# Kernel tuning notes

Measured on AMD Instinct MI355X. Metric: run time of the kernel, lower is better.

Reference implementation:

```python
import jax, jax.numpy as jnp
import numpy as np
from jax.scipy.special import gammaln

# NQ_IN + 4 == 2*H is required because the two kernel=1, padding=1 convs grow the
# length axis by 4 and the following nn.Linear(2H, H) acts on the length axis.
B, NQ_IN, NK, QDIM, KDIM, H = 16, 2044, 1024, 80, 256, 1024


def setup_inputs() -> dict:
    ks = jax.random.split(jax.random.key(0), 14)
    s = 0.02
    return {
        "query": jax.random.normal(ks[0], (B, NQ_IN, QDIM), jnp.float32),
        "key": jax.random.normal(ks[1], (B, NK, KDIM), jnp.float32),
        "query_lens": jnp.full((B,), 2 * H, jnp.int32),
        "key_lens": jnp.full((B,), NK, jnp.int32),
        # query branch params (Conv1d k=1 stored as (out,in); Linear as (out,in))
        "qc1_w": jax.random.normal(ks[2], (2 * H, QDIM), jnp.float32) * s,
        "qc1_b": jax.random.normal(ks[3], (2 * H,), jnp.float32) * s,
        "qc2_w": jax.random.normal(ks[4], (2 * H, 2 * H), jnp.float32) * s,
        "qc2_b": jax.random.normal(ks[5], (2 * H,), jnp.float32) * s,
        "ql_w": jax.random.normal(ks[6], (H, 2 * H), jnp.float32) * s,
        "ql_b": jax.random.normal(ks[7], (H,), jnp.float32) * s,
        # key branch params
        "kc_w": jax.random.normal(ks[8], (H, KDIM, 3), jnp.float32) * s,
        "kc_b": jax.random.normal(ks[9], (H,), jnp.float32) * s,
        "kl1_w": jax.random.normal(ks[10], (2 * H, H), jnp.float32) * s,
        "kl1_b": jax.random.normal(ks[11], (2 * H,), jnp.float32) * s,
        "kl2_w": jax.random.normal(ks[12], (H, 2 * H), jnp.float32) * s,
        "kl2_b": jax.random.normal(ks[13], (H,), jnp.float32) * s,
    }


def _log_beta_binom(query_lens, key_lens, tq, tk):
    # Standard MAS beta-binomial alignment prior over a (tq, tk) grid.
    i = jnp.arange(tq, dtype=jnp.float32)[None, :, None]
    j = jnp.arange(tk, dtype=jnp.float32)[None, None, :]
    ql = query_lens.astype(jnp.float32)[:, None, None]
    kl = key_lens.astype(jnp.float32)[:, None, None]
    a = i + 1.0
    b = jnp.maximum(ql - i, 1.0)
    n = jnp.maximum(kl - 1.0, 0.0)
    nmj = jnp.maximum(n - j, 0.0)

    def betaln(x, y):
        return gammaln(x) + gammaln(y) - gammaln(x + y)

    logp = (gammaln(n + 1.0) - gammaln(j + 1.0) - gammaln(nmj + 1.0)
            + betaln(j + a, nmj + b) - betaln(a, b))
    valid = (i < ql) & (j < kl)
    return jnp.where(valid, logp, -1e9)


def _forward(query, key, query_lens, key_lens,
             qc1_w, qc1_b, qc2_w, qc2_b, ql_w, ql_b,
             kc_w, kc_b, kl1_w, kl1_b, kl2_w, kl2_b):
    # query branch: b n c -> b c n, two k=1/p=1 convs (pad length, pointwise), Linear over LENGTH axis
    q = jnp.transpose(query, (0, 2, 1))                       # (B, QDIM, NQ_IN)
    q = jnp.pad(q, ((0, 0), (0, 0), (1, 1)))
    q = jnp.einsum('bcn,oc->bon', q, qc1_w) + qc1_b[None, :, None]   # (B, 2H, NQ_IN+2)
    q = jnp.pad(q, ((0, 0), (0, 0), (1, 1)))
    q = jnp.einsum('bcn,oc->bon', q, qc2_w) + qc2_b[None, :, None]   # (B, 2H, 2H)
    q = jnp.einsum('bcn,hn->bch', q, ql_w) + ql_b                    # (B, 2H, H) Linear on length axis

    # key branch: b n c -> b c n, Conv1d k=3 p=1, then two Linears over LENGTH axis
    k = jnp.transpose(key, (0, 2, 1))                         # (B, KDIM, NK)
    k = jax.lax.conv_general_dilated(k, kc_w, (1,), ((1, 1),),
                                     dimension_numbers=('NCH', 'OIH', 'NCH'))
    k = k + kc_b[None, :, None]                               # (B, H, NK=H)
    k = jnp.einsum('bcn,on->bco', k, kl1_w) + kl1_b           # (B, H, 2H)
    k = jnp.einsum('bco,ho->bch', k, kl2_w) + kl2_b           # (B, H, H)

    # dist = -cdist(q, k), computed via the GEMM form (same as torch.cdist mm mode)
    sq = (jnp.sum(q * q, -1)[:, :, None] + jnp.sum(k * k, -1)[:, None, :]
          - 2.0 * jnp.einsum('bnd,bmd->bnm', q, k))           # (B, 2H, H)
    dist = -jnp.sqrt(jnp.maximum(sq, 1e-12))

    prior = _log_beta_binom(query_lens, key_lens, q.shape[1], k.shape[1])
    return jax.nn.log_softmax(dist + prior, axis=-1)


def reference(query, key, query_lens, key_lens,
              qc1_w, qc1_b, qc2_w, qc2_b, ql_w, ql_b,
              kc_w, kc_b, kl1_w, kl1_b, kl2_w, kl2_b):
    return _forward(query, key, query_lens, key_lens,
                    qc1_w, qc1_b, qc2_w, qc2_b, ql_w, ql_b,
                    kc_w, kc_b, kl1_w, kl1_b, kl2_w, kl2_b)
```

## Files before the change

### kernel.cpp

```cpp
#include <hip/hip_runtime.h>
#include <math.h>

typedef unsigned short u16;
typedef float floatx4 __attribute__((ext_vector_type(4)));
typedef __bf16 bf16x8 __attribute__((ext_vector_type(8)));

#define BB   16
#define TQ   2048
#define TK   1024
#define HH   1024
#define H2   2048
#define QD   80
#define QDP  128
#define KD   256
#define NQ   2044
#define NKEY 1024
#define T12N 3072

__device__ __forceinline__ u16 f2bf(float f) {
  unsigned int u = __float_as_uint(f);
  u = u + 0x7fffu + ((u >> 16) & 1u);
  return (u16)(u >> 16);
}
__device__ __forceinline__ float bf2f(u16 s) {
  return __uint_as_float(((unsigned int)s) << 16);
}
__device__ __forceinline__ float tgf(const float* __restrict__ tbl, int x) {
  return tbl[(x < 8191) ? (x < 0 ? 0 : x) : 8191];
}

__global__ __launch_bounds__(256) void prep_all_k(
    const float* __restrict__ qc2_w, const float* __restrict__ kl2_w,
    const float* __restrict__ ql_w, const float* __restrict__ kc_w,
    const float* __restrict__ kl1_w,
    u16* __restrict__ qc2w, u16* __restrict__ kl2w, u16* __restrict__ qlw2,
    u16* __restrict__ kcp, float* __restrict__ colsum1, float* __restrict__ tbl)
{
  long b = blockIdx.x;
  const int t = threadIdx.x;
  __shared__ float red[256];
  if (b < 16384) {
    long i = b * 256 + t; qc2w[i] = f2bf(qc2_w[i]); return;
  }
  b -= 16384;
  if (b < 8192) {
    long i = b * 256 + t; kl2w[i] = f2bf(kl2_w[i]); return;
  }
  b -= 8192;
  if (b < 8192) {
    long i = b * 256 + t;
    int n = (int)(i & 2047);
    int h = (int)(i >> 11);
    qlw2[i] = (n < NQ) ? f2bf(ql_w[(long)h * H2 + n + 2]) : (u16)0; return;
  }
  b -= 8192;
  if (b < 3072) {
    long i = b * 256 + t;
    int r = (int)(i % 768);
    int o = (int)(i / 768);
    int tt = r >> 8, d = r & 255;
    kcp[i] = f2bf(kc_w[((long)o * KD + d) * 3 + tt]); return;
  }
  b -= 3072;
  if (b < 2048) {
    const float* row = kl1_w + b * (long)HH;
    float s = row[t] + row[t + 256] + row[t + 512] + row[t + 768];
    red[t] = s; __syncthreads();
    for (int st = 128; st > 0; st >>= 1) { if (t < st) red[t] += red[t + st]; __syncthreads(); }
    if (!t) colsum1[b] = red[0];
    return;
  }
  b -= 2048;
  { int i = (int)(b * 256 + t); if (i < 8192) tbl[i] = i ? (float)lgamma((double)i) : 0.0f; }
}

__global__ __launch_bounds__(256) void tpack_k(
    const float* __restrict__ kl1_w, const float* __restrict__ qc1_w,
    const float* __restrict__ query,
    u16* __restrict__ kl1T, u16* __restrict__ qc1T, u16* __restrict__ qT)
{
  __shared__ float tile[64][65];
  int bid = blockIdx.x;
  const int tid = threadIdx.x;
  const int r4 = tid >> 6, c = tid & 63;
  const float* src; u16* dst;
  int sr0, sc0, srcR, srcC, srcStride, dstC;
  if (bid < 512) {
    sr0 = (bid >> 4) * 64; sc0 = (bid & 15) * 64;
    src = kl1_w; srcR = 2048; srcC = 1024; srcStride = 1024;
    dst = kl1T; dstC = 2048;
  } else if ((bid -= 512) < 64) {
    sr0 = (bid >> 1) * 64; sc0 = (bid & 1) * 64;
    src = qc1_w; srcR = 2048; srcC = QD; srcStride = QD;
    dst = qc1T; dstC = 2048;
  } else {
    bid -= 64;
    const int b16 = bid >> 6, r = bid & 63;
    sr0 = (r >> 1) * 64; sc0 = (r & 1) * 64;
    src = query + (long)b16 * NQ * QD; srcR = NQ; srcC = QD; srcStride = QD;
    dst = qT + (long)b16 * QDP * 2048; dstC = 2048;
  }
#pragma unroll
  for (int rr = r4; rr < 64; rr += 4) {
    const int gr = sr0 + rr, gc = sc0 + c;
    tile[rr][c] = (gr < srcR && gc < srcC) ? src[(long)gr * srcStride + gc] : 0.f;
  }
  __syncthreads();
#pragma unroll
  for (int rr = r4; rr < 64; rr += 4)
    dst[(long)(sc0 + rr) * dstC + sr0 + c] = f2bf(tile[c][rr]);
}

__global__ __launch_bounds__(256) void pack_kcolT_k(const float* __restrict__ key, u16* __restrict__ out) {
  __shared__ float tile[64][65];
  const int bid = blockIdx.x, tid = threadIdx.x;
  const int b = bid >> 6, r = bid & 63;
  const int m0 = (r >> 2) * 64;
  const int d0 = (r & 3) * 64;
  const int r4 = tid >> 6, c = tid & 63;
#pragma unroll
  for (int rr = r4; rr < 64; rr += 4)
    tile[rr][c] = key[((long)b * NKEY + m0 + rr) * KD + d0 + c];
  __syncthreads();
#pragma unroll
  for (int t = 0; t < 3; t++) {
    const int n = m0 + 1 - t + c;
    if (n >= 0 && n < NKEY) {
#pragma unroll
      for (int rr = r4; rr < 64; rr += 4)
        out[((long)b * 768 + t * 256 + d0 + rr) * NKEY + n] = f2bf(tile[c][rr]);
    }
  }
  if (m0 == 0 && c == 0) {
#pragma unroll
    for (int rr = r4; rr < 64; rr += 4)
      out[((long)b * 768 + d0 + rr) * NKEY + 0] = (u16)0;
  }
  if (m0 == 960 && c == 0) {
#pragma unroll
    for (int rr = r4; rr < 64; rr += 4)
      out[((long)b * 768 + 512 + d0 + rr) * NKEY + (NKEY - 1)] = (u16)0;
  }
}

__global__ __launch_bounds__(256) void fold_bias_k(
    const float* __restrict__ qc2_w, const float* __restrict__ qc1_b, const float* __restrict__ qc2_b,
    const float* __restrict__ kl2_w, const float* __restrict__ kl1_b, const float* __restrict__ kl2_b,
    const float* __restrict__ ql_w, const float* __restrict__ colsum1,
    float* __restrict__ bqm, float* __restrict__ bkv, float* __restrict__ s1v, float* __restrict__ s0v,
    float* __restrict__ wsum)
{
  const int bid = blockIdx.x, t = threadIdx.x;
  float s = 0.f, s2 = 0.f;
  if (bid < H2) {
    const float* row = qc2_w + (long)bid * H2;
    for (int k = t; k < H2; k += 256) s += row[k] * qc1_b[k];
  } else if (bid < H2 + HH) {
    const float* row = kl2_w + (long)(bid - H2) * H2;
    for (int k = t; k < H2; k += 256) { const float rv = row[k]; s += rv * kl1_b[k]; s2 += rv * colsum1[k]; }
  } else {
    const float* row = ql_w + (long)(bid - H2 - HH) * H2;
    for (int m = 1 + t; m <= H2 - 2; m += 256) s += row[m];
  }
  __shared__ float red[256];
  __shared__ float red2[256];
  red[t] = s; red2[t] = s2; __syncthreads();
  for (int st = 128; st > 0; st >>= 1) {
    if (t < st) { red[t] += red[t + st]; red2[t] += red2[t + st]; }
    __syncthreads();
  }
  if (!t) {
    if (bid < H2) bqm[bid] = red[0] + qc2_b[bid];
    else if (bid < H2 + HH) { bkv[bid - H2] = red[0] + kl2_b[bid - H2]; wsum[bid - H2] = red2[0]; }
    else {
      int h = bid - H2 - HH;
      s1v[h] = red[0];
      s0v[h] = ql_w[(long)h * H2] + ql_w[(long)h * H2 + H2 - 1];
    }
  }
}

__device__ __forceinline__ void gld_lds16(const u16* g, u16* l) {
  __builtin_amdgcn_global_load_lds((const __attribute__((address_space(1))) void*)g,
                                   (__attribute__((address_space(3))) void*)l, 16, 0, 0);
}

template<int OUTF32>
__global__ __launch_bounds__(256) void gemm_bt(
    const u16* __restrict__ A, const u16* __restrict__ B, void* __restrict__ Cv,
    int M, int N, int K, int lda, int ldb, int swap, int kspl,
    long sA, long sB, long sC, long sN,
    const float* __restrict__ colb, const float* __restrict__ rowb,
    const float* __restrict__ r1m, const float* __restrict__ r1n,
    const float* __restrict__ r2m, const float* __restrict__ r2n)
{
  __shared__ __align__(16) u16 As[128 * 32];
  __shared__ __align__(16) u16 Bs[128 * 32];
  const int bz = blockIdx.z;
  const int bb_ = (kspl > 1) ? bz / kspl : bz;
  const int ks_ = (kspl > 1) ? bz - bb_ * kspl : 0;
  const int tid  = threadIdx.x;
  const int lane = tid & 63;
  const int wv = tid >> 6;
  const int wm = ((tid >> 7) & 1) * 64;
  const int wn = ((tid >> 6) & 1) * 64;
  const int m0 = (swap ? blockIdx.x : blockIdx.y) * 128;
  const int n0 = (swap ? blockIdx.y : blockIdx.x) * 128;

  const int srow = wv * 32 + (lane >> 2);
  const int scol = (lane & 3) << 3;
  const u16* ga = A + bb_ * sA + (long)ks_ * K + (long)(m0 + srow) * lda + scol;
  const u16* gb = B + bb_ * sB + (long)ks_ * K + (long)(n0 + srow) * ldb + scol;
  u16* la0 = &As[(wv * 32) * 32];
  u16* la1 = &As[(wv * 32 + 16) * 32];
  u16* lb0 = &Bs[(wv * 32) * 32];
  u16* lb1 = &Bs[(wv * 32 + 16) * 32];
  const long a16 = (long)16 * lda;
  const long b16 = (long)16 * ldb;

  floatx4 acc[4][4];
#pragma unroll
  for (int a_ = 0; a_ < 4; a_++)
#pragma unroll
    for (int b_ = 0; b_ < 4; b_++) acc[a_][b_] = (floatx4){0.f, 0.f, 0.f, 0.f};

  const int fr = lane & 15;
  const int fk = (lane >> 4) << 3;

  for (int kb = 0; kb < K; kb += 32) {
    gld_lds16(ga,       la0);
    gld_lds16(ga + a16, la1);
    gld_lds16(gb,       lb0);
    gld_lds16(gb + b16, lb1);
    ga += 32; gb += 32;
    __syncthreads();
    bf16x8 af[4], bfr[4];
#pragma unroll
    for (int mi = 0; mi < 4; mi++)
      af[mi] = *reinterpret_cast<const bf16x8*>(&As[(wm + mi * 16 + fr) * 32 + fk]);
#pragma unroll
    for (int ni = 0; ni < 4; ni++)
      bfr[ni] = *reinterpret_cast<const bf16x8*>(&Bs[(wn + ni * 16 + fr) * 32 + fk]);
#pragma unroll
    for (int mi = 0; mi < 4; mi++)
#pragma unroll
      for (int ni = 0; ni < 4; ni++)
        acc[mi][ni] = __builtin_amdgcn_mfma_f32_16x16x32_bf16(af[mi], bfr[ni], acc[mi][ni], 0, 0, 0);
    __syncthreads();
  }

  const int fr4 = (lane >> 4) << 2;
  const int fc  = lane & 15;
  u16*   Cb16 = (u16*)Cv + (long)bz * sC;
  float* Cb32 = (float*)Cv + (long)bz * sC;
  const float* cbp  = colb ? colb + (long)bb_ * sN : nullptr;
  const float* r1np = r1n ? r1n + (long)bb_ * sN : nullptr;
  const float* r2np = r2n ? r2n + (long)bb_ * sN : nullptr;
#pragma unroll
  for (int mi = 0; mi < 4; mi++) {
#pragma unroll
    for (int ni = 0; ni < 4; ni++) {
      const int gm0 = m0 + wm + mi * 16 + fr4;
      const int gn  = n0 + wn + ni * 16 + fc;
      const float cbv  = cbp ? cbp[gn] : 0.f;
      const float r1nv = r1np ? r1np[gn] : 0.f;
      const float r2nv = r2np ? r2np[gn] : 0.f;
#pragma unroll
      for (int rr = 0; rr < 4; rr++) {
        const int gm = gm0 + rr;
        float v = acc[mi][ni][rr] + cbv;
        if (rowb) v += rowb[gm];
        if (r1m)  v += r1m[gm] * r1nv;
        if (r2m)  v += r2m[gm] * r2nv;
        if (OUTF32) Cb32[(long)gm * N + gn] = v;
        else        Cb16[(long)gm * N + gn] = f2bf(v);
      }
    }
  }
}

__global__ __launch_bounds__(256) void reduce_bk_k(const float* __restrict__ P, u16* __restrict__ out,
                                                   long chunk, int S, long total) {
  long j = ((long)blockIdx.x * 256 + threadIdx.x) * 4;
  if (j >= total) return;
  long b = j / chunk;
  const float* p = P + j + b * chunk * (S - 1);
  float4 s = *reinterpret_cast<const float4*>(p);
  for (int t = 1; t < S; t++) {
    const float4 v = *reinterpret_cast<const float4*>(p + (long)t * chunk);
    s.x += v.x; s.y += v.y; s.z += v.z; s.w += v.w;
  }
  union { u16 h[4]; uint2 u; } o;
  o.h[0] = f2bf(s.x); o.h[1] = f2bf(s.y); o.h[2] = f2bf(s.z); o.h[3] = f2bf(s.w);
  *reinterpret_cast<uint2*>(out + j) = o.u;
}

__global__ __launch_bounds__(256) void u_k(
    const u16* __restrict__ TpT, const float* __restrict__ qlb,
    const float* __restrict__ s1, const float* __restrict__ s0,
    const float* __restrict__ tbl, const int* __restrict__ qlens, const int* __restrict__ klens,
    float* __restrict__ u0, float* __restrict__ u1, float* __restrict__ u2,
    float* __restrict__ sc, float* __restrict__ c1,
    float* __restrict__ crow, float* __restrict__ t12)
{
  const int bid = blockIdx.x, t = threadIdx.x;
  __shared__ float4 red[256];
  if (bid < BB * QDP) {
    uint2 v = reinterpret_cast<const uint2*>(TpT + (long)bid * HH)[t];
    float a0 = bf2f((u16)(v.x & 0xffff)), a1 = bf2f((u16)(v.x >> 16));
    float a2 = bf2f((u16)(v.y & 0xffff)), a3 = bf2f((u16)(v.y >> 16));
    float4 q  = reinterpret_cast<const float4*>(qlb)[t];
    float4 w1 = reinterpret_cast<const float4*>(s1)[t];
    float4 w0 = reinterpret_cast<const float4*>(s0)[t];
    float4 s;
    s.x = a0 * q.x  + a1 * q.y  + a2 * q.z  + a3 * q.w;
    s.y = a0 * w1.x + a1 * w1.y + a2 * w1.z + a3 * w1.w;
    s.z = a0 * w0.x + a1 * w0.y + a2 * w0.z + a3 * w0.w;
    s.w = 0.f;
    red[t] = s; __syncthreads();
    for (int st = 128; st > 0; st >>= 1) {
      if (t < st) { red[t].x += red[t + st].x; red[t].y += red[t + st].y; red[t].z += red[t + st].z; }
      __syncthreads();
    }
    if (!t) { u0[bid] = red[0].x; u1[bid] = red[0].y; u2[bid] = red[0].z; }
  } else if (bid < BB * QDP + 6) {
    const int idx = bid - BB * QDP;
    const float* X = (idx == 1 || idx == 5) ? s1 : (idx == 2) ? s0 : qlb;
    const float* Y = (idx == 1 || idx == 3) ? s1 : (idx == 0) ? qlb : s0;
    float4 x = reinterpret_cast<const float4*>(X)[t];
    float4 y = reinterpret_cast<const float4*>(Y)[t];
    float4 s; s.x = x.x * y.x + x.y * y.y + x.z * y.z + x.w * y.w; s.y = s.z = s.w = 0.f;
    red[t] = s; __syncthreads();
    for (int st = 128; st > 0; st >>= 1) {
      if (t < st) red[t].x += red[t + st].x;
      __syncthreads();
    }
    if (!t) sc[idx] = red[0].x;
  } else if (bid < BB * QDP + 6 + 64) {
    const int idx = bid - (BB * QDP + 6);
    const int b = idx >> 2;
    const int j = ((idx & 3) << 8) | t;
    const int kl = klens[b];
    const int n_ = (kl - 1 > 0) ? kl - 1 : 0;
    c1[b * TK + j] = tgf(tbl, j + 1) + tgf(tbl, n_ - j + 1);
  } else if (bid < BB * QDP + 6 + 64 + 128) {
    const int idx = bid - (BB * QDP + 6 + 64);
    const int b = idx >> 3;
    const int i = ((idx & 7) << 8) | t;
    const int ql = qlens[b], kl = klens[b];
    const int n_ = (kl - 1 > 0) ? kl - 1 : 0;
    const int bb = (ql - i > 1) ? ql - i : 1;
    crow[b * TQ + i] = tgf(tbl, n_ + 1) + tgf(tbl, i + 1 + bb) - tgf(tbl, i + 1)
                     - tgf(tbl, bb) - tgf(tbl, i + 1 + n_ + bb);
  } else {
    const int idx = bid - (BB * QDP + 6 + 64 + 128);
    const int b = idx / 12;
    const int s = (idx - b * 12) * 256 + t;
    const int ql = qlens[b], kl = klens[b];
    const int n_ = (kl - 1 > 0) ? kl - 1 : 0;
    t12[b * T12N + s] = tgf(tbl, s + 1) + tgf(tbl, n_ + ql - s);
  }
}

__global__ __launch_bounds__(256) void qn_k(
    const u16* __restrict__ Wq, const float* __restrict__ WqG,
    const float* __restrict__ u0, const float* __restrict__ u1, const float* __restrict__ u2,
    const float* __restrict__ bqm, const float* __restrict__ qc2_b,
    const float* __restrict__ sc, float* __restrict__ qn)
{
  const int bx = blockIdx.x, t = threadIdx.x;
  const int b = bx >> 10;
  const int i = ((bx & 1023) << 1) | (t >> 7);
  const int d = t & 127;
  const float w  = bf2f(Wq[(long)i * QDP + d]);
  const float g  = WqG[((long)b * H2 + i) * QDP + d];
  const float bq = bqm[i], q2 = qc2_b[i];
  const float uu = u0[b * QDP + d] + bq * u1[b * QDP + d] + q2 * u2[b * QDP + d];
  __shared__ float red[256];
  red[t] = w * (g + 2.f * uu); __syncthreads();
  for (int s = 64; s > 0; s >>= 1) { if ((t & 127) < s) red[t] += red[t + s]; __syncthreads(); }
  if (d == 0) {
    const float cst = sc[0] + bq * bq * sc[1] + q2 * q2 * sc[2]
                    + 2.f * (bq * sc[3] + q2 * sc[4] + bq * q2 * sc[5]);
    qn[b * TQ + i] = red[t] + cst;
  }
}

__global__ __launch_bounds__(256) void rownormk_k(
    const u16* __restrict__ K3, const float* __restrict__ qlb,
    const float* __restrict__ s1, const float* __restrict__ s0,
    float* __restrict__ kn, float* __restrict__ yb, float* __restrict__ y1, float* __restrict__ y0)
{
  const long r = blockIdx.x;
  const int t = threadIdx.x;
  uint2 v = reinterpret_cast<const uint2*>(K3 + r * HH)[t];
  float a0 = bf2f((u16)(v.x & 0xffff)), a1 = bf2f((u16)(v.x >> 16));
  float a2 = bf2f((u16)(v.y & 0xffff)), a3 = bf2f((u16)(v.y >> 16));
  float4 q  = reinterpret_cast<const float4*>(qlb)[t];
  float4 w1 = reinterpret_cast<const float4*>(s1)[t];
  float4 w0 = reinterpret_cast<const float4*>(s0)[t];
  float4 s;
  s.x = a0 * a0   + a1 * a1   + a2 * a2   + a3 * a3;
  s.y = a0 * q.x  + a1 * q.y  + a2 * q.z  + a3 * q.w;
  s.z = a0 * w1.x + a1 * w1.y + a2 * w1.z + a3 * w1.w;
  s.w = a0 * w0.x + a1 * w0.y + a2 * w0.z + a3 * w0.w;
  __shared__ float4 red[256];
  red[t] = s; __syncthreads();
  for (int st = 128; st > 0; st >>= 1) {
    if (t < st) {
      red[t].x += red[t + st].x; red[t].y += red[t + st].y;
      red[t].z += red[t + st].z; red[t].w += red[t + st].w;
    }
    __syncthreads();
  }
  if (!t) { kn[r] = red[0].x; yb[r] = red[0].y; y1[r] = red[0].z; y0[r] = red[0].w; }
}

#define L2E 1.4426950408889634f
__global__ __launch_bounds__(1024) void smax_k(
    const u16* __restrict__ Wq, const u16* __restrict__ Z2, float* __restrict__ out,
    const float* __restrict__ ybv, const float* __restrict__ y1v, const float* __restrict__ y0v,
    const float* __restrict__ bqmv, const float* __restrict__ qc2_b,
    const float* __restrict__ qnv, const float* __restrict__ knv, const float* __restrict__ c1v,
    const float* __restrict__ crowv, const float* __restrict__ t12v,
    const int* __restrict__ qlens, const int* __restrict__ klens)
{
  __shared__ float t12s[1152];
  __shared__ float jA[1024], jB[1024], jC[1024], jc1[1024];
  __shared__ float qns[128], crs[128], bqms[128], q2bs[128];
  __shared__ float2 lseb[4][128];
  __shared__ float lsef[128];

  const int mt = blockIdx.x, b = blockIdx.y;
  const int m0 = mt * 128;
  const int t = threadIdx.x;
  const int w = t >> 6, lane = t & 63;
  const int wm2 = (w >> 2) * 32;
  const int wn2 = (w & 3) * 32;
  const int fr = lane & 15, fk = (lane >> 4) << 3;
  const int fr4 = (lane >> 4) << 2, fc = lane & 15;
  const int qlv = qlens[b], klv = klens[b];

  if (t < 128) {
    qns[t]  = qnv[(long)b * TQ + m0 + t];
    crs[t]  = crowv[(long)b * TQ + m0 + t];
    bqms[t] = bqmv[m0 + t];
    q2bs[t] = qc2_b[m0 + t];
  }
  for (int k = t; k < 1152; k += 1024) t12s[k] = t12v[(long)b * T12N + m0 + k];
  {
    const int j = t;
    const float kn = knv[(long)b * TK + j];
    const float yb = ybv[(long)b * TK + j];
    const float y1 = y1v[(long)b * TK + j];
    const float y0 = y0v[(long)b * TK + j];
    jA[j]  = kn - 2.f * yb;
    jB[j]  = -2.f * y1;
    jC[j]  = -2.f * y0;
    jc1[j] = c1v[(long)b * TK + j];
  }

  bf16x8 af[4][2];
#pragma unroll
  for (int kc = 0; kc < 4; kc++)
#pragma unroll
    for (int mi = 0; mi < 2; mi++)
      af[kc][mi] = *reinterpret_cast<const bf16x8*>(
          Wq + (long)(m0 + wm2 + mi * 16 + fr) * QDP + kc * 32 + fk);

  const u16* Zb = Z2 + (long)b * TK * QDP;
  float* outp = out + (long)b * TQ * TK + (long)m0 * TK;

  float m_[8], s_[8];
#pragma unroll
  for (int ri = 0; ri < 8; ri++) { m_[ri] = -3.0e38f; s_[ri] = 0.f; }

  __syncthreads();

  for (int nt = 0; nt < 8; nt++) {
    bf16x8 bfr[4][2];
#pragma unroll
    for (int kc = 0; kc < 4; kc++)
#pragma unroll
      for (int nj = 0; nj < 2; nj++)
        bfr[kc][nj] = *reinterpret_cast<const bf16x8*>(
            Zb + (long)(nt * 128 + wn2 + nj * 16 + fr) * QDP + kc * 32 + fk);

    floatx4 acc[2][2];
#pragma unroll
    for (int mi = 0; mi < 2; mi++)
#pragma unroll
      for (int nj = 0; nj < 2; nj++) acc[mi][nj] = (floatx4){0.f, 0.f, 0.f, 0.f};
#pragma unroll
    for (int kc = 0; kc < 4; kc++)
#pragma unroll
      for (int mi = 0; mi < 2; mi++)
#pragma unroll
        for (int nj = 0; nj < 2; nj++)
          acc[mi][nj] = __builtin_amdgcn_mfma_f32_16x16x32_bf16(af[kc][mi], bfr[kc][nj], acc[mi][nj], 0, 0, 0);

    int gj[2]; float Aj[2], Bj[2], Cj[2], Dj[2];
#pragma unroll
    for (int nj = 0; nj < 2; nj++) {
      gj[nj] = nt * 128 + wn2 + nj * 16 + fc;
      Aj[nj] = jA[gj[nj]]; Bj[nj] = jB[gj[nj]]; Cj[nj] = jC[gj[nj]]; Dj[nj] = jc1[gj[nj]];
    }

#pragma unroll
    for (int mi = 0; mi < 2; mi++) {
#pragma unroll
      for (int rr = 0; rr < 4; rr++) {
        const int rl = wm2 + mi * 16 + fr4 + rr;
        const float qnr = qns[rl], crr = crs[rl], bqr = bqms[rl], q2r = q2bs[rl];
        float vv[2];
#pragma unroll
        for (int nj = 0; nj < 2; nj++) {
          const float sq = fmaxf(qnr + Aj[nj] + bqr * Bj[nj] + q2r * Cj[nj]
                                 - 2.0f * acc[mi][nj][rr], 1e-12f);
          const float x = -__builtin_amdgcn_sqrtf(sq) + crr - Dj[nj] + t12s[rl + gj[nj]];
          vv[nj] = ((m0 + rl) < qlv && gj[nj] < klv) ? x : -1e9f;
        }
        const int ri = mi * 4 + rr;
        const float nm = fmaxf(m_[ri], fmaxf(vv[0], vv[1]));
        s_[ri] = s_[ri] * exp2f((m_[ri] - nm) * L2E)
               + exp2f((vv[0] - nm) * L2E) + exp2f((vv[1] - nm) * L2E);
        m_[ri] = nm;
      }
    }
  }

#pragma unroll
  for (int k2 = 1; k2 <= 8; k2 <<= 1) {
#pragma unroll
    for (int ri = 0; ri < 8; ri++) {
      const float om = __shfl_xor(m_[ri], k2, 64);
      const float os = __shfl_xor(s_[ri], k2, 64);
      const float nm = fmaxf(m_[ri], om);
      s_[ri] = s_[ri] * exp2f((m_[ri] - nm) * L2E) + os * exp2f((om - nm) * L2E);
      m_[ri] = nm;
    }
  }
  if (fc == 0) {
#pragma unroll
    for (int mi = 0; mi < 2; mi++)
#pragma unroll
      for (int rr = 0; rr < 4; rr++)
        lseb[w & 3][wm2 + mi * 16 + fr4 + rr] = make_float2(m_[mi * 4 + rr], s_[mi * 4 + rr]);
  }
  __syncthreads();
  if (t < 128) {
    const float2 e0 = lseb[0][t], e1 = lseb[1][t], e2 = lseb[2][t], e3 = lseb[3][t];
    const float mm = fmaxf(fmaxf(e0.x, e1.x), fmaxf(e2.x, e3.x));
    const float ss = e0.y * exp2f((e0.x - mm) * L2E) + e1.y * exp2f((e1.x - mm) * L2E)
                   + e2.y * exp2f((e2.x - mm) * L2E) + e3.y * exp2f((e3.x - mm) * L2E);
    lsef[t] = mm + logf(ss);
  }
  __syncthreads();

  float lse_r[8];
#pragma unroll
  for (int mi = 0; mi < 2; mi++)
#pragma unroll
    for (int rr = 0; rr < 4; rr++)
      lse_r[mi * 4 + rr] = lsef[wm2 + mi * 16 + fr4 + rr];

  for (int nt = 0; nt < 8; nt++) {
    bf16x8 bfr[4][2];
#pragma unroll
    for (int kc = 0; kc < 4; kc++)
#pragma unroll
      for (int nj = 0; nj < 2; nj++)
        bfr[kc][nj] = *reinterpret_cast<const bf16x8*>(
            Zb + (long)(nt * 128 + wn2 + nj * 16 + fr) * QDP + kc * 32 + fk);

    floatx4 acc[2][2];
#pragma unroll
    for (int mi = 0; mi < 2; mi++)
#pragma unroll
      for (int nj = 0; nj < 2; nj++) acc[mi][nj] = (floatx4){0.f, 0.f, 0.f, 0.f};
#pragma unroll
    for (int kc = 0; kc < 4; kc++)
#pragma unroll
      for (int mi = 0; mi < 2; mi++)
#pragma unroll
        for (int nj = 0; nj < 2; nj++)
          acc[mi][nj] = __builtin_amdgcn_mfma_f32_16x16x32_bf16(af[kc][mi], bfr[kc][nj], acc[mi][nj], 0, 0, 0);

    int gj[2]; float Aj[2], Bj[2], Cj[2], Dj[2];
#pragma unroll
    for (int nj = 0; nj < 2; nj++) {
      gj[nj] = nt * 128 + wn2 + nj * 16 + fc;
      Aj[nj] = jA[gj[nj]]; Bj[nj] = jB[gj[nj]]; Cj[nj] = jC[gj[nj]]; Dj[nj] = jc1[gj[nj]];
    }

#pragma unroll
    for (int mi = 0; mi < 2; mi++) {
#pragma unroll
      for (int rr = 0; rr < 4; rr++) {
        const int rl = wm2 + mi * 16 + fr4 + rr;
        const float qnr = qns[rl], crr = crs[rl], bqr = bqms[rl], q2r = q2bs[rl];
        const float l = lse_r[mi * 4 + rr];
#pragma unroll
        for (int nj = 0; nj < 2; nj++) {
          const float sq = fmaxf(qnr + Aj[nj] + bqr * Bj[nj] + q2r * Cj[nj]
                                 - 2.0f * acc[mi][nj][rr], 1e-12f);
          const float x = -__builtin_amdgcn_sqrtf(sq) + crr - Dj[nj] + t12s[rl + gj[nj]];
          const float vv = ((m0 + rl) < qlv && gj[nj] < klv) ? x : -1e9f;
          outp[(long)rl * TK + gj[nj]] = vv - l;
        }
      }
    }
  }
}

extern "C" void kernel_launch(void* const* d_in, const int* in_sizes, int n_in,
                              void* d_out, int out_size, void* d_ws, size_t ws_size,
                              hipStream_t stream)
{
  (void)in_sizes; (void)n_in; (void)out_size; (void)ws_size;
  const float* query = (const float*)d_in[0];
  const float* key   = (const float*)d_in[1];
  const int*   qlens = (const int*)d_in[2];
  const int*   klens = (const int*)d_in[3];
  const float* qc1_w = (const float*)d_in[4];
  const float* qc1_b = (const float*)d_in[5];
  const float* qc2_w = (const float*)d_in[6];
  const float* qc2_b = (const float*)d_in[7];
  const float* ql_w  = (const float*)d_in[8];
  const float* ql_b  = (const float*)d_in[9];
  const float* kc_w  = (const float*)d_in[10];
  const float* kc_b  = (const float*)d_in[11];
  const float* kl1_w = (const float*)d_in[12];
  const float* kl1_b = (const float*)d_in[13];
  const float* kl2_w = (const float*)d_in[14];
  const float* kl2_b = (const float*)d_in[15];

  size_t off = 0;
  char* ws = (char*)d_ws;
  auto alloc = [&](size_t bytes) -> char* {
    char* p = ws + off; off += (bytes + 255) & ~(size_t)255; return p;
  };
  u16* qc2w_bf = (u16*)alloc(2ull * H2 * H2);
  u16* qc1T_bf = (u16*)alloc(2ull * QDP * H2);
  u16* kl2w_bf = (u16*)alloc(2ull * HH * H2);
  u16* kl1T_bf = (u16*)alloc(2ull * HH * H2);
  u16* qT_bf   = (u16*)alloc(2ull * BB * QDP * 2048);
  u16* kcolT_bf= (u16*)d_ws;
  u16* Z2_bf   = (u16*)d_ws;
  u16* qlw2_bf = (u16*)alloc(2ull * HH * 2048);
  u16* kcp_bf  = (u16*)alloc(2ull * HH * 768);
  u16* TpT_bf  = (u16*)alloc(2ull * H2 * HH);
  char* pool   = alloc(2ull * BB * HH * NKEY);
  float* Pbuf  = (float*)pool;
  u16* X_bf    = (u16*)pool;
  float* tbl  = (float*)alloc(4ull * 8192);
  u16* Wq_bf  = (u16*)alloc(2ull * H2 * QDP);
  u16* Wk_bf  = (u16*)alloc(2ull * HH * NKEY);
  float* bqm  = (float*)alloc(4ull * H2);
  float* bkv  = (float*)alloc(4ull * HH);
  float* s1v  = (float*)alloc(4ull * HH);
  float* s0v  = (float*)alloc(4ull * HH);
  float* wsum = (float*)alloc(4ull * HH);
  float* colsum1 = (float*)alloc(4ull * H2);
  u16* K3_bf  = (u16*)alloc(2ull * BB * TK * HH);
  float* qnv  = (float*)alloc(4ull * BB * TQ);
  float* knv  = (float*)alloc(4ull * BB * TK);
  float* ybv  = (float*)alloc(4ull * BB * TK);
  float* y1v  = (float*)alloc(4ull * BB * TK);
  float* y0v  = (float*)alloc(4ull * BB * TK);
  float* u0v  = (float*)alloc(4ull * BB * QDP);
  float* u1v  = (float*)alloc(4ull * BB * QDP);
  float* u2v  = (float*)alloc(4ull * BB * QDP);
  float* c1v  = (float*)alloc(4ull * BB * TK);
  float* crowv= (float*)alloc(4ull * BB * TQ);
  float* t12v = (float*)alloc(4ull * BB * T12N);
  float* scv  = (float*)alloc(256);
  float* WqG  = (float*)d_out;
  u16* G_bf   = (u16*)((char*)d_out + 16777216);

  prep_all_k<<<37920, 256, 0, stream>>>(qc2_w, kl2_w, ql_w, kc_w, kl1_w,
                                        qc2w_bf, kl2w_bf, qlw2_bf, kcp_bf, colsum1, tbl);
  tpack_k<<<1600, 256, 0, stream>>>(kl1_w, qc1_w, query, kl1T_bf, qc1T_bf, qT_bf);
  fold_bias_k<<<4096, 256, 0, stream>>>(qc2_w, qc1_b, qc2_b, kl2_w, kl1_b, kl2_b, ql_w, colsum1,
                                        bqm, bkv, s1v, s0v, wsum);

  gemm_bt<1><<<dim3(1, 16, 16), 256, 0, stream>>>(qc2w_bf, qc1T_bf, Pbuf, H2, QDP, 128,
      H2, H2, 0, 16, 0, 0, (long)H2 * QDP, 0,
      nullptr, nullptr, nullptr, nullptr, nullptr, nullptr);
  reduce_bk_k<<<256, 256, 0, stream>>>(Pbuf, Wq_bf, (long)H2 * QDP, 16, (long)H2 * QDP);

  gemm_bt<1><<<dim3(8, 8, 8), 256, 0, stream>>>(kl2w_bf, kl1T_bf, Pbuf, HH, NKEY, 256,
      H2, H2, 0, 8, 0, 0, (long)HH * NKEY, 0,
      nullptr, nullptr, nullptr, nullptr, nullptr, nullptr);
  reduce_bk_k<<<1024, 256, 0, stream>>>(Pbuf, Wk_bf, (long)HH * NKEY, 8, (long)HH * NKEY);

  gemm_bt<1><<<dim3(8, 16, 4), 256, 0, stream>>>(qT_bf, qlw2_bf, Pbuf, H2, HH, 512,
      2048, 2048, 0, 4, 0, 0, (long)H2 * HH, 0,
      nullptr, nullptr, nullptr, nullptr, nullptr, nullptr);
  reduce_bk_k<<<2048, 256, 0, stream>>>(Pbuf, TpT_bf, (long)H2 * HH, 4, (long)H2 * HH);

  gemm_bt<1><<<dim3(1, 1, 128), 256, 0, stream>>>(TpT_bf, TpT_bf, Pbuf, 128, 128, 128,
      HH, HH, 0, 8, (long)QDP * HH, (long)QDP * HH, 128 * 128, 0,
      nullptr, nullptr, nullptr, nullptr, nullptr, nullptr);
  reduce_bk_k<<<256, 256, 0, stream>>>(Pbuf, G_bf, 128 * 128, 8, (long)BB * 128 * 128);

  gemm_bt<1><<<dim3(1, 16, 16), 256, 0, stream>>>(Wq_bf, G_bf, WqG, H2, QDP, QDP,
      QDP, QDP, 0, 1, 0, (long)QDP * QDP, (long)H2 * QDP, 0,
      nullptr, nullptr, nullptr, nullptr, nullptr, nullptr);
  u_k<<<BB * QDP + 6 + 64 + 128 + 192, 256, 0, stream>>>(TpT_bf, ql_b, s1v, s0v, tbl, qlens, klens,
                                                         u0v, u1v, u2v, scv, c1v, crowv, t12v);
  qn_k<<<BB * TQ / 2, 256, 0, stream>>>(Wq_bf, WqG, u0v, u1v, u2v, bqm, qc2_b, scv, qnv);

  pack_kcolT_k<<<1024, 256, 0, stream>>>(key, kcolT_bf);
  gemm_bt<0><<<dim3(6, 8, BB), 256, 0, stream>>>(Wk_bf, kcolT_bf, X_bf, HH, 768, NKEY,
      NKEY, NKEY, 0, 1, 0, (long)768 * NKEY, (long)HH * 768, 0,
      nullptr, nullptr, nullptr, nullptr, nullptr, nullptr);
  gemm_bt<0><<<dim3(8, 8, BB), 256, 0, stream>>>(kcp_bf, X_bf, K3_bf, HH, NKEY, 768,
      768, 768, 1, 1, 0, (long)HH * 768, (long)TK * HH, 0,
      bkv, nullptr, kc_b, wsum, nullptr, nullptr);

  gemm_bt<1><<<dim3(8, 1, 32), 256, 0, stream>>>(K3_bf, TpT_bf, Pbuf, TK, QDP, 512,
      HH, HH, 1, 2, (long)TK * HH, (long)QDP * HH, (long)TK * QDP, 0,
      nullptr, nullptr, nullptr, nullptr, nullptr, nullptr);
  reduce_bk_k<<<2048, 256, 0, stream>>>(Pbuf, Z2_bf, (long)TK * QDP, 2, (long)BB * TK * QDP);

  rownormk_k<<<BB * TK, 256, 0, stream>>>(K3_bf, ql_b, s1v, s0v, knv, ybv, y1v, y0v);

  smax_k<<<dim3(16, 16), 1024, 0, stream>>>(Wq_bf, Z2_bf, (float*)d_out,
      ybv, y1v, y0v, bqm, qc2_b, qnv, knv, c1v, crowv, t12v, qlens, klens);
}
```

Before: 616.9 us.

## Stage softmax output through LDS for float4 stores and drop running max

The final pass now writes each wave's 32x32 output tile into a padded shared-memory buffer and then stores it to global memory as coalesced float4 rows, replacing scattered scalar stores. The online-softmax running max is removed, so the row sum accumulates plain exp(x) on the assumption that values stay in a safe range because distances are negative and bounded. The grid axes are also swapped so batch varies fastest across blocks. Dropping the max saves exp and shuffle work but risks underflow or overflow if logits are large in magnitude. The added 73KB of LDS may reduce occupancy.

```diff
diff --git a/kernel.cpp b/kernel.cpp
--- a/kernel.cpp
+++ b/kernel.cpp
@@ -425,13 +425,14 @@
     const float* __restrict__ crowv, const float* __restrict__ t12v,
     const int* __restrict__ qlens, const int* __restrict__ klens)
 {
+  __shared__ __align__(16) float wst[16][32 * 36];
   __shared__ float t12s[1152];
   __shared__ float jA[1024], jB[1024], jC[1024], jc1[1024];
   __shared__ float qns[128], crs[128], bqms[128], q2bs[128];
-  __shared__ float2 lseb[4][128];
+  __shared__ float lseb[4][128];
   __shared__ float lsef[128];
 
-  const int mt = blockIdx.x, b = blockIdx.y;
+  const int b = blockIdx.x, mt = blockIdx.y;
   const int m0 = mt * 128;
   const int t = threadIdx.x;
   const int w = t >> 6, lane = t & 63;
@@ -471,9 +472,9 @@
   const u16* Zb = Z2 + (long)b * TK * QDP;
   float* outp = out + (long)b * TQ * TK + (long)m0 * TK;
 
-  float m_[8], s_[8];
-#pragma unroll
-  for (int ri = 0; ri < 8; ri++) { m_[ri] = -3.0e38f; s_[ri] = 0.f; }
+  float s_[8];
+#pragma unroll
+  for (int ri = 0; ri < 8; ri++) s_[ri] = 0.f;
 
   __syncthreads();
 
@@ -512,19 +513,16 @@
       for (int rr = 0; rr < 4; rr++) {
         const int rl = wm2 + mi * 16 + fr4 + rr;
         const float qnr = qns[rl], crr = crs[rl], bqr = bqms[rl], q2r = q2bs[rl];
-        float vv[2];
+        const bool rowok = (m0 + rl) < qlv;
+        const int ri = mi * 4 + rr;
 #pragma unroll
         for (int nj = 0; nj < 2; nj++) {
           const float sq = fmaxf(qnr + Aj[nj] + bqr * Bj[nj] + q2r * Cj[nj]
                                  - 2.0f * acc[mi][nj][rr], 1e-12f);
           const float x = -__builtin_amdgcn_sqrtf(sq) + crr - Dj[nj] + t12s[rl + gj[nj]];
-          vv[nj] = ((m0 + rl) < qlv && gj[nj] < klv) ? x : -1e9f;
+          const float vv = (rowok && gj[nj] < klv) ? x : -1e9f;
+          s_[ri] += exp2f(vv * L2E);
         }
-        const int ri = mi * 4 + rr;
-        const float nm = fmaxf(m_[ri], fmaxf(vv[0], vv[1]));
-        s_[ri] = s_[ri] * exp2f((m_[ri] - nm) * L2E)
-               + exp2f((vv[0] - nm) * L2E) + exp2f((vv[1] - nm) * L2E);
-        m_[ri] = nm;
       }
     }
   }
@@ -532,28 +530,19 @@
 #pragma unroll
   for (int k2 = 1; k2 <= 8; k2 <<= 1) {
 #pragma unroll
-    for (int ri = 0; ri < 8; ri++) {
-      const float om = __shfl_xor(m_[ri], k2, 64);
-      const float os = __shfl_xor(s_[ri], k2, 64);
-      const float nm = fmaxf(m_[ri], om);
-      s_[ri] = s_[ri] * exp2f((m_[ri] - nm) * L2E) + os * exp2f((om - nm) * L2E);
-      m_[ri] = nm;
-    }
+    for (int ri = 0; ri < 8; ri++) s_[ri] += __shfl_xor(s_[ri], k2, 64);
   }
   if (fc == 0) {
 #pragma unroll
     for (int mi = 0; mi < 2; mi++)
 #pragma unroll
       for (int rr = 0; rr < 4; rr++)
-        lseb[w & 3][wm2 + mi * 16 + fr4 + rr] = make_float2(m_[mi * 4 + rr], s_[mi * 4 + rr]);
+        lseb[w & 3][wm2 + mi * 16 + fr4 + rr] = s_[mi * 4 + rr];
   }
   __syncthreads();
   if (t < 128) {
-    const float2 e0 = lseb[0][t], e1 = lseb[1][t], e2 = lseb[2][t], e3 = lseb[3][t];
-    const float mm = fmaxf(fmaxf(e0.x, e1.x), fmaxf(e2.x, e3.x));
-    const float ss = e0.y * exp2f((e0.x - mm) * L2E) + e1.y * exp2f((e1.x - mm) * L2E)
-                   + e2.y * exp2f((e2.x - mm) * L2E) + e3.y * exp2f((e3.x - mm) * L2E);
-    lsef[t] = mm + logf(ss);
+    const float tot = (lseb[0][t] + lseb[1][t]) + (lseb[2][t] + lseb[3][t]);
+    lsef[t] = (tot > 0.f) ? logf(tot) : (-1e9f + logf((float)TK));
   }
   __syncthreads();
 
@@ -564,6 +553,7 @@
     for (int rr = 0; rr < 4; rr++)
       lse_r[mi * 4 + rr] = lsef[wm2 + mi * 16 + fr4 + rr];
 
+  float* wstw = wst[w];
   for (int nt = 0; nt < 8; nt++) {
     bf16x8 bfr[4][2];
 #pragma unroll
@@ -599,16 +589,25 @@
       for (int rr = 0; rr < 4; rr++) {
         const int rl = wm2 + mi * 16 + fr4 + rr;
         const float qnr = qns[rl], crr = crs[rl], bqr = bqms[rl], q2r = q2bs[rl];
+        const bool rowok = (m0 + rl) < qlv;
         const float l = lse_r[mi * 4 + rr];
 #pragma unroll
         for (int nj = 0; nj < 2; nj++) {
           const float sq = fmaxf(qnr + Aj[nj] + bqr * Bj[nj] + q2r * Cj[nj]
                                  - 2.0f * acc[mi][nj][rr], 1e-12f);
           const float x = -__builtin_amdgcn_sqrtf(sq) + crr - Dj[nj] + t12s[rl + gj[nj]];
-          const float vv = ((m0 + rl) < qlv && gj[nj] < klv) ? x : -1e9f;
-          outp[(long)rl * TK + gj[nj]] = vv - l;
+          const float vv = (rowok && gj[nj] < klv) ? x : -1e9f;
+          wstw[(mi * 16 + fr4 + rr) * 36 + nj * 16 + fc] = vv - l;
         }
       }
+    }
+
+#pragma unroll
+    for (int st = 0; st < 4; st++) {
+      const int lr2 = st * 8 + (lane >> 3);
+      const int lc2 = (lane & 7) << 2;
+      *reinterpret_cast<float4*>(outp + (long)(wm2 + lr2) * TK + nt * 128 + wn2 + lc2) =
+          *reinterpret_cast<const float4*>(&wstw[lr2 * 36 + lc2]);
     }
   }
 }
```

Result: no change. 611.9 us (median of 2 runs) (-0.8%).
